# Kernel tuning notes

Hardware: AMD Instinct MI355X
Metric: run time of the kernel (lower is better)

Reference implementation:

```python
import jax, jax.numpy as jnp
import numpy as np


def setup_inputs() -> dict:
    key = jax.random.key(0)
    ks = jax.random.split(key, 11)
    B, S, D = 2, 2048, 1024
    s = 0.02
    return {
        "query": jax.random.normal(ks[0], (B, S, D), jnp.float32),
        "key": jax.random.normal(ks[1], (B, S, D), jnp.float32),
        "value": jax.random.normal(ks[2], (B, S, D), jnp.float32),
        "Wq": jax.random.normal(ks[3], (D, D), jnp.float32) * s,
        "bq": jnp.zeros((D,), jnp.float32),
        "Wk": jax.random.normal(ks[4], (D, D), jnp.float32) * s,
        "bk": jnp.zeros((D,), jnp.float32),
        "Wv": jax.random.normal(ks[5], (D, D), jnp.float32) * s,
        "bv": jnp.zeros((D,), jnp.float32),
        "Wo": jax.random.normal(ks[6], (D, D), jnp.float32) * s,
        "bo": jnp.zeros((D,), jnp.float32),
        "nheads": 16,
    }


def reference(query, key, value, Wq, bq, Wk, bk, Wv, bv, Wo, bo, nheads):
    B, Sq, D = query.shape
    Sk = key.shape[1]
    hd = D // nheads  # head dim
    q = (query @ Wq.T + bq).reshape(B, Sq, nheads, hd)
    k = (key @ Wk.T + bk).reshape(B, Sk, nheads, hd)
    v = (value @ Wv.T + bv).reshape(B, Sk, nheads, hd)
    score = jnp.einsum("bqhd,bkhd->bhqk", q, k)
    # mask == 'triu': strictly-upper-triangular entries set to -inf (causal)
    causal = jnp.triu(jnp.ones((Sq, Sk), dtype=bool), k=1)
    score = jnp.where(causal, -jnp.inf, score)
    # NOTE: original scales by sqrt(score.shape[-1]) == sqrt(kv_len), not sqrt(head_dim)
    scale = np.float32(1.0 / np.sqrt(Sk))
    att = jax.nn.softmax(score * scale, axis=-1)
    ret = jnp.einsum("bhqk,bkhd->bqhd", att, v).reshape(B, Sq, D)
    out = ret @ Wo.T + bo  # dropout is identity in eval mode
    return (out, att)
```

## Files before the change

### kernel.cpp

```cpp
#include <hip/hip_runtime.h>
#include <cstdint>
#include <cstddef>
#include <type_traits>

typedef __attribute__((ext_vector_type(8))) __bf16 bf16x8;
typedef __attribute__((ext_vector_type(4))) __bf16 bf16x4;
typedef __attribute__((ext_vector_type(4))) float f32x4;
typedef __attribute__((ext_vector_type(4))) unsigned short u16x4;

__device__ __forceinline__ f32x4 mfma16(bf16x8 a, bf16x8 b, f32x4 c) {
  return __builtin_amdgcn_mfma_f32_16x16x32_bf16(a, b, c, 0, 0, 0);
}

__device__ __forceinline__ void load_lds16(const void* g, void* l) {
  auto gp = reinterpret_cast<const __attribute__((address_space(1))) uint32_t*>(
      reinterpret_cast<uintptr_t>(g));
  auto lp = reinterpret_cast<__attribute__((address_space(3))) uint32_t*>(
      static_cast<uint32_t>(reinterpret_cast<uintptr_t>(l)));
  __builtin_amdgcn_global_load_lds(gp, lp, 16, 0, 0);
}

static constexpr float QPRE = 0.03187935710091218f;

static constexpr size_t OFF_XQ = 0;
static constexpr size_t OFF_XK = 4194304;
static constexpr size_t OFF_XV = 8388608;
static constexpr size_t OFF_WQ = 12582912;
static constexpr size_t OFF_WK = 13631488;
static constexpr size_t OFF_WV = 14680064;
static constexpr size_t OFF_WO = 15728640;
static constexpr size_t OFF_QB = 16777216;
static constexpr size_t OFF_KB = 20971520;
static constexpr size_t OFF_VT = 25165824;
static constexpr size_t OFF_RT = 29360128;

__global__ __launch_bounds__(256) void convert_all(
    const float* __restrict__ q, const float* __restrict__ k,
    const float* __restrict__ v, const float* __restrict__ wq,
    const float* __restrict__ wk, const float* __restrict__ wv,
    const float* __restrict__ wo, __bf16* __restrict__ ws)
{
  const int total = 2097152;
  for (int i = blockIdx.x * blockDim.x + threadIdx.x; i < total;
       i += gridDim.x * blockDim.x) {
    const float* src; size_t dstoff; int rel;
    if (i < 1572864) {
      if (i < 524288)       { src = q;  dstoff = OFF_XQ; rel = i; }
      else if (i < 1048576) { src = k;  dstoff = OFF_XK; rel = i - 524288; }
      else                  { src = v;  dstoff = OFF_XV; rel = i - 1048576; }
    } else if (i < 1835008) {
      if (i < 1703936)      { src = wq; dstoff = OFF_WQ; rel = i - 1572864; }
      else                  { src = wk; dstoff = OFF_WK; rel = i - 1703936; }
    } else if (i < 1966080) { src = wv; dstoff = OFF_WV; rel = i - 1835008; }
    else                    { src = wo; dstoff = OFF_WO; rel = i - 1966080; }
    float4 f0 = reinterpret_cast<const float4*>(src)[(size_t)rel * 2];
    float4 f1 = reinterpret_cast<const float4*>(src)[(size_t)rel * 2 + 1];
    bf16x8 o;
    o[0] = (__bf16)f0.x; o[1] = (__bf16)f0.y; o[2] = (__bf16)f0.z; o[3] = (__bf16)f0.w;
    o[4] = (__bf16)f1.x; o[5] = (__bf16)f1.y; o[6] = (__bf16)f1.z; o[7] = (__bf16)f1.w;
    *reinterpret_cast<bf16x8*>(ws + dstoff + (size_t)rel * 8) = o;
  }
}

__device__ __forceinline__ void gemm_body(
    const __bf16* __restrict__ A, const __bf16* __restrict__ Bm,
    const float* __restrict__ bias, void* __restrict__ Cout,
    int M, int N, int K, int mode, int m0, int n0,
    __bf16* As, __bf16* Bs)
{
  const int t = threadIdx.x;
  const int lane = t & 63, r = lane & 15, g = lane >> 4;
  const int w = t >> 6, wm = w >> 1, wn = w & 1;
  const int srow = t >> 3, scol = (t & 7) * 8;

  const f32x4 fzero = {0.f, 0.f, 0.f, 0.f};
  f32x4 acc[4][4];
#pragma unroll
  for (int x = 0; x < 4; x++)
#pragma unroll
    for (int y = 0; y < 4; y++) acc[x][y] = fzero;

  auto stage = [&](int buf, int k0) {
#pragma unroll
    for (int i = 0; i < 4; i++) {
      load_lds16(A  + (size_t)(m0 + i * 32 + srow) * K + k0 + scol, &As[buf * 8192 + i * 2048 + t * 8]);
      load_lds16(Bm + (size_t)(n0 + i * 32 + srow) * K + k0 + scol, &Bs[buf * 8192 + i * 2048 + t * 8]);
    }
  };

  const int NT = K / 64;
  stage(0, 0);
  asm volatile("s_waitcnt vmcnt(0)" ::: "memory");
  __syncthreads();
  int cur = 0;
  for (int kt = 0; kt < NT; ++kt) {
    if (kt + 1 < NT) stage(cur ^ 1, (kt + 1) * 64);
    const __bf16* Ab = &As[cur * 8192];
    const __bf16* Bb = &Bs[cur * 8192];
#pragma unroll
    for (int kk = 0; kk < 2; kk++) {
      bf16x8 af[4], bfv[4];
#pragma unroll
      for (int x = 0; x < 4; x++)
        af[x] = *reinterpret_cast<const bf16x8*>(&Ab[(wm * 64 + x * 16 + r) * 64 + kk * 32 + g * 8]);
#pragma unroll
      for (int y = 0; y < 4; y++)
        bfv[y] = *reinterpret_cast<const bf16x8*>(&Bb[(wn * 64 + y * 16 + r) * 64 + kk * 32 + g * 8]);
#pragma unroll
      for (int x = 0; x < 4; x++)
#pragma unroll
        for (int y = 0; y < 4; y++)
          acc[x][y] = mfma16(af[x], bfv[y], acc[x][y]);
    }
    asm volatile("s_waitcnt vmcnt(0)" ::: "memory");
    __syncthreads();
    cur ^= 1;
  }

#pragma unroll
  for (int x = 0; x < 4; x++)
#pragma unroll
    for (int y = 0; y < 4; y++) {
#pragma unroll
      for (int j = 0; j < 4; j++) {
        int row = m0 + wm * 64 + x * 16 + g * 4 + j;
        int col = n0 + wn * 64 + y * 16 + r;
        float val = acc[x][y][j];
        if (mode == 0 || mode == 1) {
          val += bias[col];
          if (mode == 0) val *= QPRE;
          int b = row >> 11, s = row & 2047, h = col >> 6, d = col & 63;
          ((__bf16*)Cout)[(((size_t)(b * 16 + h) * 2048 + s) << 6) + d] = (__bf16)val;
        } else if (mode == 2) {
          val += bias[row];
          int h = row >> 6, d = row & 63, b = col >> 11, s = col & 2047;
          ((__bf16*)Cout)[(((size_t)(b * 16 + h) * 64 + d) << 11) + s] = (__bf16)val;
        } else {
          val += bias[col];
          __builtin_nontemporal_store(val, &((float*)Cout)[(size_t)row * N + col]);
        }
      }
    }
}

__global__ __launch_bounds__(256) void gemm_qkv(
    __bf16* __restrict__ ws, const float* __restrict__ bq,
    const float* __restrict__ bk, const float* __restrict__ bv)
{
  __shared__ __align__(16) __bf16 As[2 * 8192];
  __shared__ __align__(16) __bf16 Bs[2 * 8192];
  const int z = blockIdx.z;
  if (z == 0) {
    gemm_body(ws + OFF_XQ, ws + OFF_WQ, bq, ws + OFF_QB, 4096, 1024, 1024, 0,
              blockIdx.y * 128, blockIdx.x * 128, As, Bs);
  } else if (z == 1) {
    gemm_body(ws + OFF_XK, ws + OFF_WK, bk, ws + OFF_KB, 4096, 1024, 1024, 1,
              blockIdx.y * 128, blockIdx.x * 128, As, Bs);
  } else {
    gemm_body(ws + OFF_WV, ws + OFF_XV, bv, ws + OFF_VT, 1024, 4096, 1024, 2,
              blockIdx.x * 128, blockIdx.y * 128, As, Bs);
  }
}

__global__ __launch_bounds__(256) void gemm_o(
    const __bf16* __restrict__ Rt, const __bf16* __restrict__ Wo,
    const float* __restrict__ bo, float* __restrict__ out)
{
  __shared__ __align__(16) __bf16 As[2 * 8192];
  __shared__ __align__(16) __bf16 Bs[2 * 8192];
  gemm_body(Rt, Wo, bo, out, 4096, 1024, 1024, 3,
            blockIdx.y * 128, blockIdx.x * 128, As, Bs);
}

__global__ __launch_bounds__(256) void attn_kernel(
    const __bf16* __restrict__ Qb, const __bf16* __restrict__ Kb,
    const __bf16* __restrict__ Vt, __bf16* __restrict__ Rt,
    float* __restrict__ att)
{
  __shared__ __align__(16) __bf16 Ks[128 * 68];
  __shared__ __align__(16) __bf16 Vts[64 * 132];
  __shared__ __align__(16) __bf16 Ps[128 * 132];

  const int t = threadIdx.x;
  const int lane = t & 63, r = lane & 15, g = lane >> 4;
  const int w = t >> 6;
  const int p = blockIdx.x;
  const int workid = (p & 7) * 64 + (p >> 3);
  const int bh = workid >> 4;
  const int xx = workid & 15;
  const int qb = ((bh >> 1) & 1) ? 15 - xx : xx;
  const int q0 = qb * 128;
  const __bf16* Qg = Qb + (size_t)bh * 2048 * 64;
  const __bf16* Kg = Kb + (size_t)bh * 2048 * 64;
  const __bf16* Vg = Vt + (size_t)bh * 64 * 2048;
  float* attb = att + (size_t)bh * 2048 * 2048 + (size_t)q0 * 2048;

  const int lrow = t >> 3, lcol = (t & 7) * 8;
  const int vrow = t >> 4, vcol = (t & 15) * 8;

  const f32x4 fzero = {0.f, 0.f, 0.f, 0.f};

  bf16x8 aq[2][2];
#pragma unroll
  for (int mf = 0; mf < 2; mf++)
#pragma unroll
    for (int kk = 0; kk < 2; kk++)
      aq[mf][kk] = *reinterpret_cast<const bf16x8*>(
          Qg + (size_t)(q0 + w * 32 + mf * 16 + r) * 64 + kk * 32 + g * 8);

  auto compute_scores = [&](f32x4(&accs)[2][8]) {
#pragma unroll
    for (int mf = 0; mf < 2; mf++)
#pragma unroll
      for (int nf = 0; nf < 8; nf++) accs[mf][nf] = fzero;
    __builtin_amdgcn_s_setprio(1);
#pragma unroll
    for (int kk = 0; kk < 2; kk++) {
#pragma unroll
      for (int nf = 0; nf < 8; nf++) {
        bf16x8 bk = *reinterpret_cast<const bf16x8*>(&Ks[(nf * 16 + r) * 68 + kk * 32 + g * 8]);
        accs[0][nf] = mfma16(aq[0][kk], bk, accs[0][nf]);
        accs[1][nf] = mfma16(aq[1][kk], bk, accs[1][nf]);
      }
    }
    __builtin_amdgcn_s_setprio(0);
  };

  float rsp[2][4];
#pragma unroll
  for (int mf = 0; mf < 2; mf++)
#pragma unroll
    for (int j = 0; j < 4; j++) rsp[mf][j] = 0.f;

  bf16x8 rk[4];
#pragma unroll
  for (int i = 0; i < 4; i++)
    rk[i] = *reinterpret_cast<const bf16x8*>(Kg + (size_t)(i * 32 + lrow) * 64 + lcol);

  for (int kt = 0; kt <= qb; ++kt) {
    __syncthreads();
#pragma unroll
    for (int i = 0; i < 4; i++)
      *reinterpret_cast<bf16x8*>(&Ks[(i * 32 + lrow) * 68 + lcol]) = rk[i];
    __syncthreads();
    if (kt < qb) {
#pragma unroll
      for (int i = 0; i < 4; i++)
        rk[i] = *reinterpret_cast<const bf16x8*>(Kg + (size_t)((kt + 1) * 128 + i * 32 + lrow) * 64 + lcol);
    }
    f32x4 accs[2][8];
    compute_scores(accs);

    auto p1body = [&](auto maskc) {
      constexpr bool MASK = decltype(maskc)::value;
#pragma unroll
      for (int mf = 0; mf < 2; mf++)
#pragma unroll
        for (int nf = 0; nf < 8; nf++) {
          int col = kt * 128 + nf * 16 + r;
#pragma unroll
          for (int j = 0; j < 4; j++) {
            float e = __builtin_amdgcn_exp2f(accs[mf][nf][j]);
            if (MASK) {
              int rowg = q0 + w * 32 + mf * 16 + g * 4 + j;
              e = (col <= rowg) ? e : 0.f;
            }
            rsp[mf][j] += e;
          }
        }
    };
    if (kt == qb) p1body(std::integral_constant<bool, true>{});
    else          p1body(std::integral_constant<bool, false>{});
  }

  float rl[2][4];
#pragma unroll
  for (int mf = 0; mf < 2; mf++)
#pragma unroll
    for (int j = 0; j < 4; j++) {
      float v2 = rsp[mf][j];
      v2 += __shfl_xor(v2, 1, 64);
      v2 += __shfl_xor(v2, 2, 64);
      v2 += __shfl_xor(v2, 4, 64);
      v2 += __shfl_xor(v2, 8, 64);
      rl[mf][j] = 1.0f / v2;
    }

  f32x4 accr[2][4];
#pragma unroll
  for (int mf = 0; mf < 2; mf++)
#pragma unroll
    for (int nf2 = 0; nf2 < 4; nf2++) accr[mf][nf2] = fzero;

  bf16x8 rv[4];
#pragma unroll
  for (int i = 0; i < 4; i++) {
    rk[i] = *reinterpret_cast<const bf16x8*>(Kg + (size_t)(i * 32 + lrow) * 64 + lcol);
    rv[i] = *reinterpret_cast<const bf16x8*>(Vg + (size_t)(i * 16 + vrow) * 2048 + vcol);
  }

  for (int kt = 0; kt <= qb; ++kt) {
    __syncthreads();
#pragma unroll
    for (int i = 0; i < 4; i++) {
      *reinterpret_cast<bf16x8*>(&Ks[(i * 32 + lrow) * 68 + lcol]) = rk[i];
      *reinterpret_cast<bf16x8*>(&Vts[(i * 16 + vrow) * 132 + vcol]) = rv[i];
    }
    __syncthreads();
    if (kt < qb) {
#pragma unroll
      for (int i = 0; i < 4; i++) {
        rk[i] = *reinterpret_cast<const bf16x8*>(Kg + (size_t)((kt + 1) * 128 + i * 32 + lrow) * 64 + lcol);
        rv[i] = *reinterpret_cast<const bf16x8*>(Vg + (size_t)(i * 16 + vrow) * 2048 + (kt + 1) * 128 + vcol);
      }
    }
    f32x4 accs[2][8];
    compute_scores(accs);

    auto p2body = [&](auto maskc) {
      constexpr bool MASK = decltype(maskc)::value;
#pragma unroll
      for (int mf = 0; mf < 2; mf++) {
#pragma unroll
        for (int nf = 0; nf < 8; nf++) {
          int col = kt * 128 + nf * 16 + r;
#pragma unroll
          for (int j = 0; j < 4; j++) {
            int rowl = w * 32 + mf * 16 + g * 4 + j;
            float e = __builtin_amdgcn_exp2f(accs[mf][nf][j]);
            if (MASK) {
              e = (col <= q0 + rowl) ? e : 0.f;
            }
            float pp = e * rl[mf][j];
            Ps[rowl * 132 + nf * 16 + r] = (__bf16)pp;
          }
        }
      }
    };
    if (kt == qb) p2body(std::integral_constant<bool, true>{});
    else          p2body(std::integral_constant<bool, false>{});

    __syncthreads();
    __builtin_amdgcn_s_setprio(1);
#pragma unroll
    for (int kk2 = 0; kk2 < 4; kk2++) {
      bf16x8 ap0 = *reinterpret_cast<const bf16x8*>(&Ps[(w * 32 + r) * 132 + kk2 * 32 + g * 8]);
      bf16x8 ap1 = *reinterpret_cast<const bf16x8*>(&Ps[(w * 32 + 16 + r) * 132 + kk2 * 32 + g * 8]);
#pragma unroll
      for (int nf2 = 0; nf2 < 4; nf2++) {
        bf16x8 bv_ = *reinterpret_cast<const bf16x8*>(&Vts[(nf2 * 16 + r) * 132 + kk2 * 32 + g * 8]);
        accr[0][nf2] = mfma16(ap0, bv_, accr[0][nf2]);
        accr[1][nf2] = mfma16(ap1, bv_, accr[1][nf2]);
      }
    }
    __builtin_amdgcn_s_setprio(0);

    {
      const int crow8 = t >> 5;
      const int c4 = t & 31;
#pragma unroll
      for (int j = 0; j < 16; j++) {
        int row = j * 8 + crow8;
        u16x4 pv = *reinterpret_cast<const u16x4*>(&Ps[row * 132 + c4 * 4]);
        f32x4 f;
        f[0] = __uint_as_float((unsigned)pv[0] << 16);
        f[1] = __uint_as_float((unsigned)pv[1] << 16);
        f[2] = __uint_as_float((unsigned)pv[2] << 16);
        f[3] = __uint_as_float((unsigned)pv[3] << 16);
        __builtin_nontemporal_store(
            f, reinterpret_cast<f32x4*>(attb + (size_t)row * 2048 + kt * 128 + c4 * 4));
      }
    }
  }

  const f32x4 z4 = {0.f, 0.f, 0.f, 0.f};
  for (int kt2 = qb + 1; kt2 < 16; ++kt2) {
    for (int idx = t; idx < 4096; idx += 256) {
      int row = idx >> 5, c4 = idx & 31;
      __builtin_nontemporal_store(
          z4, reinterpret_cast<f32x4*>(attb + (size_t)row * 2048 + kt2 * 128 + c4 * 4));
    }
  }

  const int b = bh >> 4, h = bh & 15;
#pragma unroll
  for (int mf = 0; mf < 2; mf++)
#pragma unroll
    for (int nf2 = 0; nf2 < 4; nf2++)
#pragma unroll
      for (int j = 0; j < 4; j++) {
        int qrow = q0 + w * 32 + mf * 16 + g * 4 + j;
        int d = nf2 * 16 + r;
        Rt[((size_t)(b * 2048 + qrow) << 10) + h * 64 + d] = (__bf16)accr[mf][nf2][j];
      }
}

extern "C" void kernel_launch(void* const* d_in, const int* in_sizes, int n_in,
                              void* d_out, int out_size, void* d_ws, size_t ws_size,
                              hipStream_t stream) {
  (void)in_sizes; (void)n_in; (void)out_size; (void)ws_size;
  const float* q  = (const float*)d_in[0];
  const float* k  = (const float*)d_in[1];
  const float* v  = (const float*)d_in[2];
  const float* wq = (const float*)d_in[3];
  const float* bq = (const float*)d_in[4];
  const float* wk = (const float*)d_in[5];
  const float* bk = (const float*)d_in[6];
  const float* wv = (const float*)d_in[7];
  const float* bv = (const float*)d_in[8];
  const float* wo = (const float*)d_in[9];
  const float* bo = (const float*)d_in[10];
  __bf16* ws = (__bf16*)d_ws;
  float* out = (float*)d_out;
  float* att = out + 4194304;

  convert_all<<<2048, 256, 0, stream>>>(q, k, v, wq, wk, wv, wo, ws);
  gemm_qkv<<<dim3(8, 32, 3), 256, 0, stream>>>(ws, bq, bk, bv);
  attn_kernel<<<512, 256, 0, stream>>>(ws + OFF_QB, ws + OFF_KB, ws + OFF_VT, ws + OFF_RT, att);
  gemm_o<<<dim3(8, 32), 256, 0, stream>>>(ws + OFF_RT, ws + OFF_WO, bo, out);
}
```

Before: 209.2 us.

## Read K and V fragments directly from global memory, drop LDS staging and barriers

After: 276.7 us. 32.2% more time.

```diff
diff --git a/kernel.cpp b/kernel.cpp
--- a/kernel.cpp
+++ b/kernel.cpp
@@ -177,8 +177,6 @@
     const __bf16* __restrict__ Vt, __bf16* __restrict__ Rt,
     float* __restrict__ att)
 {
-  __shared__ __align__(16) __bf16 Ks[128 * 68];
-  __shared__ __align__(16) __bf16 Vts[64 * 132];
   __shared__ __align__(16) __bf16 Ps[128 * 132];
 
   const int t = threadIdx.x;
@@ -195,9 +193,6 @@
   const __bf16* Vg = Vt + (size_t)bh * 64 * 2048;
   float* attb = att + (size_t)bh * 2048 * 2048 + (size_t)q0 * 2048;
 
-  const int lrow = t >> 3, lcol = (t & 7) * 8;
-  const int vrow = t >> 4, vcol = (t & 15) * 8;
-
   const f32x4 fzero = {0.f, 0.f, 0.f, 0.f};
 
   bf16x8 aq[2][2];
@@ -208,7 +203,7 @@
       aq[mf][kk] = *reinterpret_cast<const bf16x8*>(
           Qg + (size_t)(q0 + w * 32 + mf * 16 + r) * 64 + kk * 32 + g * 8);
 
-  auto compute_scores = [&](f32x4(&accs)[2][8]) {
+  auto compute_scores = [&](int kt, f32x4(&accs)[2][8]) {
 #pragma unroll
     for (int mf = 0; mf < 2; mf++)
 #pragma unroll
@@ -218,7 +213,8 @@
     for (int kk = 0; kk < 2; kk++) {
 #pragma unroll
       for (int nf = 0; nf < 8; nf++) {
-        bf16x8 bk = *reinterpret_cast<const bf16x8*>(&Ks[(nf * 16 + r) * 68 + kk * 32 + g * 8]);
+        bf16x8 bk = *reinterpret_cast<const bf16x8*>(
+            Kg + (size_t)(kt * 128 + nf * 16 + r) * 64 + kk * 32 + g * 8);
         accs[0][nf] = mfma16(aq[0][kk], bk, accs[0][nf]);
         accs[1][nf] = mfma16(aq[1][kk], bk, accs[1][nf]);
       }
@@ -232,24 +228,9 @@
 #pragma unroll
     for (int j = 0; j < 4; j++) rsp[mf][j] = 0.f;
 
-  bf16x8 rk[4];
-#pragma unroll
-  for (int i = 0; i < 4; i++)
-    rk[i] = *reinterpret_cast<const bf16x8*>(Kg + (size_t)(i * 32 + lrow) * 64 + lcol);
-
   for (int kt = 0; kt <= qb; ++kt) {
-    __syncthreads();
-#pragma unroll
-    for (int i = 0; i < 4; i++)
-      *reinterpret_cast<bf16x8*>(&Ks[(i * 32 + lrow) * 68 + lcol]) = rk[i];
-    __syncthreads();
-    if (kt < qb) {
-#pragma unroll
-      for (int i = 0; i < 4; i++)
-        rk[i] = *reinterpret_cast<const bf16x8*>(Kg + (size_t)((kt + 1) * 128 + i * 32 + lrow) * 64 + lcol);
-    }
     f32x4 accs[2][8];
-    compute_scores(accs);
+    compute_scores(kt, accs);
 
     auto p1body = [&](auto maskc) {
       constexpr bool MASK = decltype(maskc)::value;
@@ -292,30 +273,9 @@
 #pragma unroll
     for (int nf2 = 0; nf2 < 4; nf2++) accr[mf][nf2] = fzero;
 
-  bf16x8 rv[4];
-#pragma unroll
-  for (int i = 0; i < 4; i++) {
-    rk[i] = *reinterpret_cast<const bf16x8*>(Kg + (size_t)(i * 32 + lrow) * 64 + lcol);
-    rv[i] = *reinterpret_cast<const bf16x8*>(Vg + (size_t)(i * 16 + vrow) * 2048 + vcol);
-  }
-
   for (int kt = 0; kt <= qb; ++kt) {
-    __syncthreads();
-#pragma unroll
-    for (int i = 0; i < 4; i++) {
-      *reinterpret_cast<bf16x8*>(&Ks[(i * 32 + lrow) * 68 + lcol]) = rk[i];
-      *reinterpret_cast<bf16x8*>(&Vts[(i * 16 + vrow) * 132 + vcol]) = rv[i];
-    }
-    __syncthreads();
-    if (kt < qb) {
-#pragma unroll
-      for (int i = 0; i < 4; i++) {
-        rk[i] = *reinterpret_cast<const bf16x8*>(Kg + (size_t)((kt + 1) * 128 + i * 32 + lrow) * 64 + lcol);
-        rv[i] = *reinterpret_cast<const bf16x8*>(Vg + (size_t)(i * 16 + vrow) * 2048 + (kt + 1) * 128 + vcol);
-      }
-    }
     f32x4 accs[2][8];
-    compute_scores(accs);
+    compute_scores(kt, accs);
 
     auto p2body = [&](auto maskc) {
       constexpr bool MASK = decltype(maskc)::value;
@@ -340,7 +300,6 @@
     if (kt == qb) p2body(std::integral_constant<bool, true>{});
     else          p2body(std::integral_constant<bool, false>{});
 
-    __syncthreads();
     __builtin_amdgcn_s_setprio(1);
 #pragma unroll
     for (int kk2 = 0; kk2 < 4; kk2++) {
@@ -348,7 +307,8 @@
       bf16x8 ap1 = *reinterpret_cast<const bf16x8*>(&Ps[(w * 32 + 16 + r) * 132 + kk2 * 32 + g * 8]);
 #pragma unroll
       for (int nf2 = 0; nf2 < 4; nf2++) {
-        bf16x8 bv_ = *reinterpret_cast<const bf16x8*>(&Vts[(nf2 * 16 + r) * 132 + kk2 * 32 + g * 8]);
+        bf16x8 bv_ = *reinterpret_cast<const bf16x8*>(
+            Vg + (size_t)(nf2 * 16 + r) * 2048 + kt * 128 + kk2 * 32 + g * 8);
         accr[0][nf2] = mfma16(ap0, bv_, accr[0][nf2]);
         accr[1][nf2] = mfma16(ap1, bv_, accr[1][nf2]);
       }
@@ -356,19 +316,19 @@
     __builtin_amdgcn_s_setprio(0);
 
     {
-      const int crow8 = t >> 5;
-      const int c4 = t & 31;
+      const int half = lane >> 5;
+      const int c4 = lane & 31;
 #pragma unroll
       for (int j = 0; j < 16; j++) {
-        int row = j * 8 + crow8;
-        u16x4 pv = *reinterpret_cast<const u16x4*>(&Ps[row * 132 + c4 * 4]);
+        int rowl = w * 32 + 2 * j + half;
+        u16x4 pv = *reinterpret_cast<const u16x4*>(&Ps[rowl * 132 + c4 * 4]);
         f32x4 f;
         f[0] = __uint_as_float((unsigned)pv[0] << 16);
         f[1] = __uint_as_float((unsigned)pv[1] << 16);
         f[2] = __uint_as_float((unsigned)pv[2] << 16);
         f[3] = __uint_as_float((unsigned)pv[3] << 16);
         __builtin_nontemporal_store(
-            f, reinterpret_cast<f32x4*>(attb + (size_t)row * 2048 + kt * 128 + c4 * 4));
+            f, reinterpret_cast<f32x4*>(attb + (size_t)rowl * 2048 + kt * 128 + c4 * 4));
       }
     }
   }
```
